# Kernel tuning notes

Hardware: AMD Instinct MI355X
Metric: run time of the kernel (lower is better)

## Reference

```python
import jax, jax.numpy as jnp
import numpy as np
from jax import lax

EPS = 1e-5  # torch BatchNorm2d default eps


def _bn_relu_conv_res(x, g, bt, m, v, W, b):
    # x: (B,C,h,w). Eval-mode BN + ReLU + 3x3 'same' conv + residual (per region tile).
    y = (x - m[:, None, None]) * (g * lax.rsqrt(v + EPS))[:, None, None] + bt[:, None, None]
    y = jax.nn.relu(y)
    y = lax.conv_general_dilated(y, W, (1, 1), ((1, 1), (1, 1)),
                                 dimension_numbers=('NCHW', 'OIHW', 'NCHW'))
    return y + b[None, :, None, None] + x

_tile_fn = jax.vmap(_bn_relu_conv_res)  # vmap over the leading tile axis


def _flat77(p):
    return p[:7, :7].reshape((49,) + p.shape[2:])


def _region_layer(x, g, bt, m, v, W, b):
    # grid=(8,8): torch.split(split_size=H//7) -> 7 tiles of size s and one remainder tile r per axis.
    B, C, H, _ = x.shape
    s = H // 7          # 18 for H=132
    r = H - 7 * s       # 6
    # interior 7x7 tiles (s x s), batched in one vmapped conv
    xi = x[:, :, :7 * s, :7 * s].reshape(B, C, 7, s, 7, s).transpose(2, 4, 0, 1, 3, 5).reshape(49, B, C, s, s)
    oi = _tile_fn(xi, _flat77(g), _flat77(bt), _flat77(m), _flat77(v), _flat77(W), _flat77(b))
    oi = oi.reshape(7, 7, B, C, s, s).transpose(2, 3, 0, 4, 1, 5).reshape(B, C, 7 * s, 7 * s)
    # right column tiles (s x r), j = 7
    xr = x[:, :, :7 * s, 7 * s:].reshape(B, C, 7, s, r).transpose(2, 0, 1, 3, 4)
    orr = _tile_fn(xr, g[:7, 7], bt[:7, 7], m[:7, 7], v[:7, 7], W[:7, 7], b[:7, 7])
    orr = orr.transpose(1, 2, 0, 3, 4).reshape(B, C, 7 * s, r)
    # bottom row tiles (r x s), i = 7
    xb = x[:, :, 7 * s:, :7 * s].reshape(B, C, r, 7, s).transpose(3, 0, 1, 2, 4)
    ob = _tile_fn(xb, g[7, :7], bt[7, :7], m[7, :7], v[7, :7], W[7, :7], b[7, :7])
    ob = ob.transpose(1, 2, 3, 0, 4).reshape(B, C, r, 7 * s)
    # corner tile (r x r)
    oc = _bn_relu_conv_res(x[:, :, 7 * s:, 7 * s:], g[7, 7], bt[7, 7], m[7, 7], v[7, 7], W[7, 7], b[7, 7])
    return jnp.concatenate([jnp.concatenate([oi, orr], 3), jnp.concatenate([ob, oc], 3)], 2)


def _conv(x, W, b, stride):
    y = lax.conv_general_dilated(x, W, (stride, stride), 'VALID',
                                 dimension_numbers=('NCHW', 'OIHW', 'NCHW'))
    return y + b[None, :, None, None]


def _maxpool2(x):
    return lax.reduce_window(x, -jnp.inf, lax.max, (1, 1, 2, 2), (1, 1, 2, 2), 'VALID')


def _bn(x, g, bt, m, v):
    return (x - m[:, None, None]) * (g * lax.rsqrt(v + EPS))[:, None, None] + bt[:, None, None]


def _forward(x, conv1_w, conv1_b, rg_g, rg_b, rg_m, rg_v, rg_w, rg_cb,
             bn2_g, bn2_b, bn2_m, bn2_v, conv2_w, conv2_b, conv3_w, conv3_b,
             conv4_w, conv4_b, conv5_w, conv5_b, fc1_w, fc1_b, fc2_w, fc2_b, fc3_w, fc3_b):
    h = _conv(x, conv1_w, conv1_b, 1)                 # (B,32,132,132)
    h = _region_layer(h, rg_g, rg_b, rg_m, rg_v, rg_w, rg_cb)
    h = jax.nn.relu(h)
    h = _maxpool2(h)                                  # (B,32,66,66)
    h = _bn(h, bn2_g, bn2_b, bn2_m, bn2_v)
    h = jax.nn.relu(_conv(h, conv2_w, conv2_b, 1))    # (B,16,59,59)
    h = jax.nn.relu(_conv(h, conv3_w, conv3_b, 1))    # (B,16,52,52)
    h = jax.nn.relu(_conv(h, conv4_w, conv4_b, 2))    # (B,16,24,24)
    h = jax.nn.relu(_conv(h, conv5_w, conv5_b, 1))    # (B,16,20,20)
    h = h.reshape(h.shape[0], -1)                     # (B,6400)
    h = jax.nn.relu(h @ fc1_w.T + fc1_b)              # dropout = identity (eval)
    h = jax.nn.relu(h @ fc2_w.T + fc2_b)
    return h @ fc3_w.T + fc3_b                        # (B,12)


def setup_inputs() -> dict:
    key = jax.random.key(0)
    ks = jax.random.split(key, 32)
    n = lambda i, shape, s=0.05: s * jax.random.normal(ks[i], shape, jnp.float32)
    B = 64
    return {
        'x': jax.random.normal(ks[0], (B, 3, 142, 142), jnp.float32),
        'conv1_w': n(1, (32, 3, 11, 11)),
        'conv1_b': n(2, (32,), 0.01),
        'rg_g': 1.0 + n(3, (8, 8, 32), 0.1),
        'rg_b': n(4, (8, 8, 32), 0.1),
        'rg_m': n(5, (8, 8, 32), 0.1),
        'rg_v': 1.0 + n(6, (8, 8, 32), 0.1),
        'rg_w': n(7, (8, 8, 32, 32, 3, 3)),
        'rg_cb': n(8, (8, 8, 32), 0.01),
        'bn2_g': 1.0 + n(9, (32,), 0.1),
        'bn2_b': n(10, (32,), 0.1),
        'bn2_m': n(11, (32,), 0.1),
        'bn2_v': 1.0 + n(12, (32,), 0.1),
        'conv2_w': n(13, (16, 32, 8, 8)),
        'conv2_b': n(14, (16,), 0.01),
        'conv3_w': n(15, (16, 16, 8, 8)),
        'conv3_b': n(16, (16,), 0.01),
        'conv4_w': n(17, (16, 16, 6, 6)),
        'conv4_b': n(18, (16,), 0.01),
        'conv5_w': n(19, (16, 16, 5, 5)),
        'conv5_b': n(20, (16,), 0.01),
        'fc1_w': n(21, (4096, 6400), 0.01),
        'fc1_b': n(22, (4096,), 0.01),
        'fc2_w': n(23, (2048, 4096), 0.01),
        'fc2_b': n(24, (2048,), 0.01),
        'fc3_w': n(25, (12, 2048), 0.01),
        'fc3_b': n(26, (12,), 0.01),
    }


def reference(x, conv1_w, conv1_b, rg_g, rg_b, rg_m, rg_v, rg_w, rg_cb,
              bn2_g, bn2_b, bn2_m, bn2_v, conv2_w, conv2_b, conv3_w, conv3_b,
              conv4_w, conv4_b, conv5_w, conv5_b, fc1_w, fc1_b, fc2_w, fc2_b, fc3_w, fc3_b):
    return _forward(x, conv1_w, conv1_b, rg_g, rg_b, rg_m, rg_v, rg_w, rg_cb,
                    bn2_g, bn2_b, bn2_m, bn2_v, conv2_w, conv2_b, conv3_w, conv3_b,
                    conv4_w, conv4_b, conv5_w, conv5_b, fc1_w, fc1_b, fc2_w, fc2_b, fc3_w, fc3_b)
```

## Files before the change

### kernel.cpp

```cpp
#include <hip/hip_runtime.h>

#define EPS 1e-5f

typedef __attribute__((ext_vector_type(4)))  __bf16 bf16x4;
typedef __attribute__((ext_vector_type(8)))  __bf16 bf16x8;
typedef __attribute__((ext_vector_type(4)))  float  f32x4;
typedef __attribute__((ext_vector_type(16))) float  f32x16;

template <int TH, int TW, int NIMG>
__device__ void fused_body(const float* __restrict__ xg,
                           const float* __restrict__ c1w, const float* __restrict__ c1b,
                           const float* __restrict__ gg, const float* __restrict__ bb,
                           const float* __restrict__ mm, const float* __restrict__ vv,
                           const float* __restrict__ ww, const float* __restrict__ cbp,
                           const float* __restrict__ g2, const float* __restrict__ b2,
                           const float* __restrict__ m2, const float* __restrict__ v2,
                           __bf16* __restrict__ hp,
                           __bf16* act, __bf16* wlds1, __bf16* sx, __bf16* zbuf,
                           float* prm,
                           int reg, int n0, int Y0, int X0)
{
    constexpr int C     = TW + 10;
    constexpr int RR    = TH + 10;
    constexpr int SSTR  = 4 * (TH + 11);
    constexpr int NP    = TH * TW;
    constexpr int NPT   = (NP + 31) / 32;
    constexpr int NT    = (NPT + 3) / 4;
    constexpr int PWW   = TW / 2;
    constexpr int TOT   = 3 * RR * C;
    constexpr int NLOAD = (TOT + 255) / 256;

    const int tid  = threadIdx.x;
    const int lane = tid & 63;
    const int wv   = tid >> 6;
    const int half = lane >> 5;
    const int l31  = lane & 31;
    const int YP = Y0 >> 1, XP = X0 >> 1;

    if (tid < 32) {
        const float sc = gg[reg * 32 + tid] * rsqrtf(vv[reg * 32 + tid] + EPS);
        const float b1 = c1b[tid];
        prm[tid]       = sc;
        prm[32 + tid]  = bb[reg * 32 + tid] - mm[reg * 32 + tid] * sc + sc * b1;
        prm[64 + tid]  = cbp[reg * 32 + tid] + b1;
        const float s2 = g2[tid] * rsqrtf(v2[tid] + EPS);
        prm[96 + tid]  = s2;
        prm[128 + tid] = b2[tid] - m2[tid] * s2;
    }
    for (int i = tid; i < 16896; i += 256) {
        const int j = i & 7, co = (i >> 3) & 31, hf = (i >> 8) & 1, cc = i >> 9;
        const int c = cc % 3, kx = cc / 3;
        const int k48 = c * 16 + hf * 8 + j, ky = k48 >> 2, ci = k48 & 3;
        const float v = (ci < 3 && ky < 11) ? c1w[((co * 3 + ci) * 11 + ky) * 11 + kx] : 0.f;
        wlds1[i] = (__bf16)v;
    }
    for (int i = tid; i < 9216; i += 256) {
        const int co = i / 288, r = i - co * 288;
        const int ci = r / 9, tap = r - ci * 9;
        act[((tap * 4 + (ci >> 3)) * 32 + co) * 8 + (ci & 7)] = (__bf16)ww[(long)reg * 9216 + i];
    }
    for (int i = tid; i < C * SSTR; i += 256) sx[i] = (__bf16)0.f;
    __syncthreads();

    bf16x8 afrag[18];
    #pragma unroll
    for (int c = 0; c < 18; ++c) {
        const int tap = c >> 1;
        const int grp = (c & 1) * 2 + half;
        afrag[c] = *(const bf16x8*)&act[((tap * 4 + grp) * 32 + l31) * 8];
    }

    const int sub = l31 & 3;
    int py[NT], px[NT], yy0[NT], xx0[NT]; bool val[NT];
    #pragma unroll
    for (int t = 0; t < NT; ++t) {
        const int til = wv + t * 4;
        int p = til * 32 + l31;
        val[t] = (til < NPT) && (p < NP);
        if (!val[t]) p = l31;
        const int q = p >> 2;
        py[t] = q / PWW; px[t] = q - py[t] * PWW;
        yy0[t] = 2 * py[t] + ((p & 3) >> 1);
        xx0[t] = 2 * px[t] + (p & 1);
    }

    float pf[NLOAD];
    #pragma unroll
    for (int k = 0; k < NLOAD; ++k) {
        const int idx = tid + k * 256;
        float v = 0.f;
        if (idx < TOT) {
            const int col = idx % C, rr = idx / C;
            const int row = rr % RR, ci = rr / RR;
            v = xg[(((long)n0 * 3 + ci) * 142 + Y0 + row) * 142 + X0 + col];
        }
        pf[k] = v;
    }
    __syncthreads();

    for (int img = 0; img < NIMG; ++img) {
        const int n = n0 + img;
        #pragma unroll
        for (int k = 0; k < NLOAD; ++k) {
            const int idx = tid + k * 256;
            if (idx < TOT) {
                const int col = idx % C, rr = idx / C;
                const int row = rr % RR, ci = rr / RR;
                sx[col * SSTR + row * 4 + ci] = (__bf16)pf[k];
            }
        }
        __syncthreads();
        if (img + 1 < NIMG) {
            #pragma unroll
            for (int k = 0; k < NLOAD; ++k) {
                const int idx = tid + k * 256;
                if (idx < TOT) {
                    const int col = idx % C, rr = idx / C;
                    const int row = rr % RR, ci = rr / RR;
                    pf[k] = xg[(((long)(n + 1) * 3 + ci) * 142 + Y0 + row) * 142 + X0 + col];
                }
            }
        }
        f32x16 a1[NT];
        #pragma unroll
        for (int t = 0; t < NT; ++t) a1[t] = (f32x16){};
        for (int kx = 0; kx < 11; ++kx) {
            #pragma unroll
            for (int c = 0; c < 3; ++c) {
                const bf16x8 A = *(const bf16x8*)&wlds1[(((kx * 3 + c) * 2 + half) * 32 + l31) * 8];
                #pragma unroll
                for (int t = 0; t < NT; ++t) {
                    if (wv + t * 4 < NPT) {
                        const int off = (xx0[t] + kx) * SSTR + (yy0[t] + c * 4 + half * 2) * 4;
                        const bf16x4 lo = *(const bf16x4*)&sx[off];
                        const bf16x4 hi = *(const bf16x4*)&sx[off + 4];
                        a1[t] = __builtin_amdgcn_mfma_f32_32x32x16_bf16(
                                    A, __builtin_shufflevector(lo, hi, 0, 1, 2, 3, 4, 5, 6, 7),
                                    a1[t], 0, 0, 0);
                    }
                }
            }
        }
        #pragma unroll
        for (int t = 0; t < NT; ++t) {
            if (val[t]) {
                const int pix = yy0[t] * TW + xx0[t];
                #pragma unroll
                for (int g = 0; g < 4; ++g) {
                    bf16x4 pk;
                    #pragma unroll
                    for (int j = 0; j < 4; ++j) {
                        const int co = 4 * half + 8 * g + j;
                        pk[j] = (__bf16)fmaxf(a1[t][4 * g + j] * prm[co] + prm[32 + co], 0.f);
                    }
                    *(bf16x4*)&act[pix * 36 + 8 * g + 4 * half] = pk;
                }
            }
        }
        __syncthreads();
        f32x16 ar[NT];
        #pragma unroll
        for (int t = 0; t < NT; ++t) ar[t] = a1[t];
        #pragma unroll
        for (int c = 0; c < 18; ++c) {
            const int tap = c >> 1;
            const int ky = tap / 3, kxx = tap - ky * 3;
            #pragma unroll
            for (int t = 0; t < NT; ++t) {
                if (wv + t * 4 < NPT) {
                    const int yy = yy0[t] + ky - 1, xx = xx0[t] + kxx - 1;
                    const bool in = ((unsigned)yy < (unsigned)TH) && ((unsigned)xx < (unsigned)TW);
                    const __bf16* src = in ? &act[(yy * TW + xx) * 36 + (c & 1) * 16 + half * 8] : zbuf;
                    const bf16x4 lo = *(const bf16x4*)src;
                    const bf16x4 hi = *(const bf16x4*)(src + 4);
                    ar[t] = __builtin_amdgcn_mfma_f32_32x32x16_bf16(
                                afrag[c], __builtin_shufflevector(lo, hi, 0, 1, 2, 3, 4, 5, 6, 7),
                                ar[t], 0, 0, 0);
                }
            }
        }
        #pragma unroll
        for (int t = 0; t < NT; ++t) {
            if (wv + t * 4 < NPT) {
                #pragma unroll
                for (int r = 0; r < 16; ++r) {
                    const int co = (r & 3) + 8 * (r >> 2) + 4 * half;
                    float v = ar[t][r] + prm[64 + co];
                    v = fmaxf(v, 0.f);
                    v = fmaxf(v, __shfl_xor(v, 1));
                    v = fmaxf(v, __shfl_xor(v, 2));
                    if (val[t] && sub == 0) {
                        hp[(((long)n * 32 + co) * 66 + YP + py[t]) * 66 + XP + px[t]]
                            = (__bf16)(v * prm[96 + co] + prm[128 + co]);
                    }
                }
            }
        }
    }
}

__global__ __launch_bounds__(256, 2) void k_fused(const float* __restrict__ xg,
                                                  const float* __restrict__ c1w,
                                                  const float* __restrict__ c1b,
                                                  const float* __restrict__ gg,
                                                  const float* __restrict__ bb,
                                                  const float* __restrict__ mm,
                                                  const float* __restrict__ vv,
                                                  const float* __restrict__ ww,
                                                  const float* __restrict__ cbp,
                                                  const float* __restrict__ g2,
                                                  const float* __restrict__ b2,
                                                  const float* __restrict__ m2,
                                                  const float* __restrict__ v2,
                                                  __bf16* __restrict__ hp)
{
    __shared__ __align__(16) __bf16 act[11664];
    __shared__ __align__(16) __bf16 wlds1[16896];
    __shared__ __align__(16) __bf16 sx[3248];
    __shared__ __align__(16) __bf16 zbuf[8];
    __shared__ float prm[160];
    if (threadIdx.x < 8) zbuf[threadIdx.x] = (__bf16)0.f;
    const int reg = blockIdx.x;
    const int ri = reg >> 3, rj = reg & 7;
    const int n0 = blockIdx.y * 8;
    const int Y0 = ri * 18, X0 = rj * 18;
    if (ri < 7 && rj < 7)
        fused_body<18, 18, 8>(xg, c1w, c1b, gg, bb, mm, vv, ww, cbp, g2, b2, m2, v2, hp,
                              act, wlds1, sx, zbuf, prm, reg, n0, Y0, X0);
    else if (ri < 7)
        fused_body<18, 6, 8>(xg, c1w, c1b, gg, bb, mm, vv, ww, cbp, g2, b2, m2, v2, hp,
                             act, wlds1, sx, zbuf, prm, reg, n0, Y0, X0);
    else if (rj < 7)
        fused_body<6, 18, 8>(xg, c1w, c1b, gg, bb, mm, vv, ww, cbp, g2, b2, m2, v2, hp,
                             act, wlds1, sx, zbuf, prm, reg, n0, Y0, X0);
    else
        fused_body<6, 6, 8>(xg, c1w, c1b, gg, bb, mm, vv, ww, cbp, g2, b2, m2, v2, hp,
                            act, wlds1, sx, zbuf, prm, reg, n0, Y0, X0);
}

__global__ void k_wprep(const float* __restrict__ w, __bf16* __restrict__ wA,
                        int CIN, int KS, int NCHUNK)
{
    const int NG = CIN / 16;
    const int total = NG * NCHUNK * 512;
    const int i = blockIdx.x * 256 + threadIdx.x;
    if (i >= total) return;
    const int j   = i & 7;
    const int co  = (i >> 3) & 15;
    const int quad = (i >> 7) & 3;
    const int ch  = (i >> 9) % NCHUNK;
    const int g   = (i >> 9) / NCHUNK;
    const int k   = ch * 32 + quad * 8 + j;
    const int t   = k >> 4, c = k & 15;
    float v = 0.f;
    if (t < KS * KS) v = w[((co * CIN + g * 16 + c) * KS + t / KS) * KS + t % KS];
    wA[i] = (__bf16)v;
}

template <typename TIN, typename TOUT, int CIN, int KS, int HIN, int HOUT, int R>
__global__ __launch_bounds__(256) void k_conv_mfma(const TIN* __restrict__ in,
                                                   const __bf16* __restrict__ wA,
                                                   const float* __restrict__ bias,
                                                   TOUT* __restrict__ out)
{
    constexpr int NG     = CIN / 16;
    constexpr int TAPS   = KS * KS;
    constexpr int NCHUNK = (TAPS * 16 + 31) / 32;
    constexpr int NROWS  = R + KS - 1;
    constexpr int NP     = R * HOUT;
    constexpr int NTIL   = (NP + 15) / 16;
    constexpr int NT     = (NTIL + 3) / 4;
    __shared__ __align__(16) __bf16 act[NROWS * HIN * 20];
    __shared__ __align__(16) __bf16 wl[NCHUNK * 512];
    const int tid  = threadIdx.x;
    const int lane = tid & 63;
    const int wv   = tid >> 6;
    const int quad = lane >> 4;
    const int m    = lane & 15;
    const int n    = blockIdx.y;
    int y0 = blockIdx.x * R; if (y0 > HOUT - R) y0 = HOUT - R;

    int yl[NT], xx[NT]; bool val[NT];
    #pragma unroll
    for (int t = 0; t < NT; ++t) {
        const int til = wv + t * 4;
        int p = til * 16 + m;
        val[t] = (til < NTIL) && (p < NP);
        if (!val[t]) p = m;
        yl[t] = p / HOUT; xx[t] = p - yl[t] * HOUT;
    }
    f32x4 acc[NT];
    #pragma unroll
    for (int t = 0; t < NT; ++t) acc[t] = (f32x4){0.f, 0.f, 0.f, 0.f};

    for (int g = 0; g < NG; ++g) {
        if (g) __syncthreads();
        for (int i = tid; i < NCHUNK * 256; i += 256)
            ((unsigned*)wl)[i] = ((const unsigned*)wA)[g * NCHUNK * 256 + i];
        for (int i = tid; i < 16 * NROWS * HIN; i += 256) {
            const int c = i / (NROWS * HIN), px = i - c * (NROWS * HIN);
            const int r = px / HIN, xc = px - r * HIN;
            act[px * 20 + c] = (__bf16)in[(((long)n * CIN + g * 16 + c) * HIN + y0 + r) * HIN + xc];
        }
        __syncthreads();
        for (int ch = 0; ch < NCHUNK; ++ch) {
            const bf16x8 a = *(const bf16x8*)&wl[(ch * 4 + quad) * 128 + m * 8];
            const int kbase = ch * 32 + quad * 8;
            int t = kbase >> 4;
            const int c0 = kbase & 15;
            int ky = 0, kx = 0;
            if (t < TAPS) { ky = t / KS; kx = t - ky * KS; }
            #pragma unroll
            for (int tt = 0; tt < NT; ++tt) {
                const int off = ((yl[tt] + ky) * HIN + xx[tt] + kx) * 20 + c0;
                const bf16x4 lo = *(const bf16x4*)&act[off];
                const bf16x4 hi = *(const bf16x4*)&act[off + 4];
                const bf16x8 b = __builtin_shufflevector(lo, hi, 0, 1, 2, 3, 4, 5, 6, 7);
                acc[tt] = __builtin_amdgcn_mfma_f32_16x16x32_bf16(a, b, acc[tt], 0, 0, 0);
            }
        }
    }
    #pragma unroll
    for (int tt = 0; tt < NT; ++tt) {
        if (!val[tt]) continue;
        #pragma unroll
        for (int r = 0; r < 4; ++r) {
            const int co = quad * 4 + r;
            out[(((long)n * 16 + co) * HOUT + y0 + yl[tt]) * HOUT + xx[tt]]
                = (TOUT)fmaxf(acc[tt][r] + bias[co], 0.f);
        }
    }
}

template <int CIN, int KS, int STRIDE, int HIN, int HOUT>
__global__ __launch_bounds__(256) void k_conv(const float* __restrict__ in,
                                              const float* __restrict__ w,
                                              const float* __restrict__ bias,
                                              __bf16* __restrict__ out)
{
    const int co = blockIdx.y, n = blockIdx.z;
    constexpr int GR  = (HOUT + 3) / 4;
    constexpr int WSZ = CIN * KS * KS;
    constexpr int LEN = KS + 3 * STRIDE;
    __shared__ float ws[WSZ];
    for (int i = threadIdx.x; i < WSZ; i += 256) ws[i] = w[co * WSZ + i];
    __syncthreads();
    const int g = blockIdx.x * 256 + threadIdx.x;
    if (g >= HOUT * GR) return;
    const int y = g / GR;
    int x0 = (g - y * GR) * 4;
    if (x0 > HOUT - 4) x0 = HOUT - 4;
    float a0 = bias[co], a1 = a0, a2 = a0, a3 = a0;
    const float* base = in + (long)n * CIN * HIN * HIN;
    for (int ci = 0; ci < CIN; ++ci) {
        for (int ky = 0; ky < KS; ++ky) {
            const float* row = base + ((long)ci * HIN + y * STRIDE + ky) * HIN + x0 * STRIDE;
            float r[LEN];
            #pragma unroll
            for (int i = 0; i < LEN; ++i) r[i] = row[i];
            const float* wr = ws + (ci * KS + ky) * KS;
            #pragma unroll
            for (int kx = 0; kx < KS; ++kx) {
                const float wv = wr[kx];
                a0 = fmaf(wv, r[kx],              a0);
                a1 = fmaf(wv, r[kx + STRIDE],     a1);
                a2 = fmaf(wv, r[kx + 2 * STRIDE], a2);
                a3 = fmaf(wv, r[kx + 3 * STRIDE], a3);
            }
        }
    }
    __bf16* o = out + (((long)n * 16 + co) * HOUT + y) * HOUT + x0;
    o[0] = (__bf16)fmaxf(a0, 0.f); o[1] = (__bf16)fmaxf(a1, 0.f);
    o[2] = (__bf16)fmaxf(a2, 0.f); o[3] = (__bf16)fmaxf(a3, 0.f);
}

__global__ __launch_bounds__(256) void k_fc2(const float* __restrict__ A,
                                             const float* __restrict__ W,
                                             float* __restrict__ C,
                                             int N, int K, int kchunk)
{
    __shared__ float As[64][68];
    __shared__ float Bs[64][132];
    const int n0 = blockIdx.x * 128;
    const int kbeg = blockIdx.y * kchunk;
    const int tid = threadIdx.x;
    const int tm = tid >> 4, tn = tid & 15;
    const int am = tid >> 2, ac = tid & 3;
    const int bn = tid >> 1, bh = tid & 1;
    float acc[4][8] = {};
    for (int k0 = kbeg; k0 < kbeg + kchunk; k0 += 64) {
        #pragma unroll
        for (int q = 0; q < 4; ++q) {
            const int kk = ac * 16 + q * 4;
            const float4 v = *(const float4*)&A[(long)am * K + k0 + kk];
            As[kk + 0][am] = v.x; As[kk + 1][am] = v.y;
            As[kk + 2][am] = v.z; As[kk + 3][am] = v.w;
        }
        const int nn = n0 + bn;
        if (nn < N) {
            #pragma unroll
            for (int q = 0; q < 8; ++q) {
                const int kk = bh * 32 + q * 4;
                const float4 v = *(const float4*)&W[(long)nn * K + k0 + kk];
                Bs[kk + 0][bn] = v.x; Bs[kk + 1][bn] = v.y;
                Bs[kk + 2][bn] = v.z; Bs[kk + 3][bn] = v.w;
            }
        }
        __syncthreads();
        #pragma unroll 4
        for (int kk = 0; kk < 64; ++kk) {
            float a[4], b[8];
            #pragma unroll
            for (int i = 0; i < 4; ++i) a[i] = As[kk][tm * 4 + i];
            #pragma unroll
            for (int j = 0; j < 8; ++j) b[j] = Bs[kk][tn * 8 + j];
            #pragma unroll
            for (int i = 0; i < 4; ++i)
                #pragma unroll
                for (int j = 0; j < 8; ++j)
                    acc[i][j] = fmaf(a[i], b[j], acc[i][j]);
        }
        __syncthreads();
    }
    #pragma unroll
    for (int i = 0; i < 4; ++i) {
        const int m = tm * 4 + i;
        #pragma unroll
        for (int j = 0; j < 8; ++j) {
            const int nn = n0 + tn * 8 + j;
            if (nn < N) atomicAdd(&C[(long)m * N + nn], acc[i][j]);
        }
    }
}

__global__ __launch_bounds__(256) void k_bias_act(const float* __restrict__ C,
                                                  const float* __restrict__ bias,
                                                  float* __restrict__ out,
                                                  int N, int total, int relu)
{
    const int i = blockIdx.x * 256 + threadIdx.x;
    if (i >= total) return;
    float v = C[i] + bias[i % N];
    if (relu) v = fmaxf(v, 0.f);
    out[i] = v;
}

extern "C" void kernel_launch(void* const* d_in, const int* in_sizes, int n_in,
                              void* d_out, int out_size, void* d_ws, size_t ws_size,
                              hipStream_t stream)
{
    (void)in_sizes; (void)n_in; (void)out_size; (void)ws_size;
    const float* x       = (const float*)d_in[0];
    const float* conv1_w = (const float*)d_in[1];
    const float* conv1_b = (const float*)d_in[2];
    const float* rg_g    = (const float*)d_in[3];
    const float* rg_b    = (const float*)d_in[4];
    const float* rg_m    = (const float*)d_in[5];
    const float* rg_v    = (const float*)d_in[6];
    const float* rg_w    = (const float*)d_in[7];
    const float* rg_cb   = (const float*)d_in[8];
    const float* bn2_g   = (const float*)d_in[9];
    const float* bn2_b   = (const float*)d_in[10];
    const float* bn2_m   = (const float*)d_in[11];
    const float* bn2_v   = (const float*)d_in[12];
    const float* conv2_w = (const float*)d_in[13];
    const float* conv2_b = (const float*)d_in[14];
    const float* conv3_w = (const float*)d_in[15];
    const float* conv3_b = (const float*)d_in[16];
    const float* conv4_w = (const float*)d_in[17];
    const float* conv4_b = (const float*)d_in[18];
    const float* conv5_w = (const float*)d_in[19];
    const float* conv5_b = (const float*)d_in[20];
    const float* fc1_w   = (const float*)d_in[21];
    const float* fc1_b   = (const float*)d_in[22];
    const float* fc2_w   = (const float*)d_in[23];
    const float* fc2_b   = (const float*)d_in[24];
    const float* fc3_w   = (const float*)d_in[25];
    const float* fc3_b   = (const float*)d_in[26];

    float* ws = (float*)d_ws;
    __bf16* hp  = (__bf16*)ws;
    float*  b2f = ws + 4460544;
    __bf16* wA2 = (__bf16*)(b2f);
    __bf16* wA3 = (__bf16*)(b2f + 16384);
    __bf16* wA5 = (__bf16*)(b2f + 24576);
    __bf16* h3  = (__bf16*)(b2f + 27904);
    float*  h4  = b2f + 27904 + 1782272;
    __bf16* h5  = (__bf16*)(h4 + 2768896);
    float*  h6  = (float*)h5 + 294912;
    float*  f1  = h6 + 409600;
    float*  f2  = f1 + 262144;
    float*  f3  = f2 + 131072;

    k_fused<<<dim3(64, 8), 256, 0, stream>>>(x, conv1_w, conv1_b,
                                             rg_g, rg_b, rg_m, rg_v, rg_w, rg_cb,
                                             bn2_g, bn2_b, bn2_m, bn2_v, hp);

    k_wprep<<<dim3(128), 256, 0, stream>>>(conv2_w, wA2, 32, 8, 32);
    k_wprep<<<dim3(64), 256, 0, stream>>>(conv3_w, wA3, 16, 8, 32);
    k_wprep<<<dim3(26), 256, 0, stream>>>(conv5_w, wA5, 16, 5, 13);

    k_conv_mfma<__bf16, __bf16, 32, 8, 66, 59, 4><<<dim3(15, 64), 256, 0, stream>>>(hp, wA2, conv2_b, h3);
    k_conv_mfma<__bf16, float, 16, 8, 59, 52, 4><<<dim3(13, 64), 256, 0, stream>>>(h3, wA3, conv3_b, h4);
    k_conv<16, 6, 2, 52, 24><<<dim3(1, 16, 64), 256, 0, stream>>>(h4, conv4_w, conv4_b, h5);
    k_conv_mfma<__bf16, float, 16, 5, 24, 20, 10><<<dim3(2, 64), 256, 0, stream>>>(h5, wA5, conv5_b, h6);

    hipMemsetAsync(f1, 0, 262144 * sizeof(float), stream);
    k_fc2<<<dim3(32, 10), 256, 0, stream>>>(h6, fc1_w, f1, 4096, 6400, 640);
    k_bias_act<<<dim3((262144 + 255) / 256), 256, 0, stream>>>(f1, fc1_b, f1, 4096, 262144, 1);

    hipMemsetAsync(f2, 0, 131072 * sizeof(float), stream);
    k_fc2<<<dim3(16, 16), 256, 0, stream>>>(f1, fc2_w, f2, 2048, 4096, 256);
    k_bias_act<<<dim3((131072 + 255) / 256), 256, 0, stream>>>(f2, fc2_b, f2, 2048, 131072, 1);

    hipMemsetAsync(f3, 0, 768 * sizeof(float), stream);
    k_fc2<<<dim3(1, 16), 256, 0, stream>>>(f2, fc3_w, f3, 12, 2048, 128);
    k_bias_act<<<dim3(3), 256, 0, stream>>>(f3, fc3_b, (float*)d_out, 12, 768, 0);
}
```

Before: 751.9 us.

## Precompute all weights once, switch intermediates to channels-last, cut LDS and raise occupancy

Adds one k_wprep_all kernel that converts the conv1, region, conv2, conv3 and conv5 weights into MFMA-ready bf16 layouts in global memory. The fused and conv kernels now read A fragments directly from global/L1 instead of staging them in LDS, which frees shared memory and lets launch bounds ask for 4 blocks per CU. The fused kernel's pooled output and conv2's output become channels-last so the next conv can do 16-byte vector loads, and LDS strides are padded to 40 and 24 so B operands load as single bf16x8. Images per fused block drop from 8 to 4 (more blocks), and conv5 rows per block drop from 10 to 5. The risks are extra global-memory weight reads inside the MFMA loops and register pressure under the tighter launch bounds.

After: 766.9 us. +2.0%, slower.

```diff
diff --git a/kernel.cpp b/kernel.cpp
--- a/kernel.cpp
+++ b/kernel.cpp
@@ -7,17 +7,67 @@
 typedef __attribute__((ext_vector_type(4)))  float  f32x4;
 typedef __attribute__((ext_vector_type(16))) float  f32x16;
 
+__device__ inline void wprep_generic(const float* __restrict__ w, __bf16* __restrict__ wA,
+                                     int CIN, int KS, int NCHUNK, int i)
+{
+    const int j    = i & 7;
+    const int co   = (i >> 3) & 15;
+    const int quad = (i >> 7) & 3;
+    const int ch   = (i >> 9) % NCHUNK;
+    const int g    = (i >> 9) / NCHUNK;
+    const int k    = ch * 32 + quad * 8 + j;
+    const int t    = k >> 4, c = k & 15;
+    float v = 0.f;
+    if (t < KS * KS) v = w[((co * CIN + g * 16 + c) * KS + t / KS) * KS + t % KS];
+    wA[i] = (__bf16)v;
+}
+
+__global__ __launch_bounds__(256) void k_wprep_all(const float* __restrict__ c1w,
+                                                   const float* __restrict__ rgw,
+                                                   const float* __restrict__ w2,
+                                                   const float* __restrict__ w3,
+                                                   const float* __restrict__ w5,
+                                                   __bf16* __restrict__ wA1,
+                                                   __bf16* __restrict__ wR,
+                                                   __bf16* __restrict__ wA2,
+                                                   __bf16* __restrict__ wA3,
+                                                   __bf16* __restrict__ wA5)
+{
+    int i = blockIdx.x * 256 + threadIdx.x;
+    if (i < 16896) {
+        const int j = i & 7, co = (i >> 3) & 31, hf = (i >> 8) & 1, grp = i >> 9;
+        const int kx = grp / 3, c = grp - kx * 3;
+        const int k48 = c * 16 + hf * 8 + j, ky = k48 >> 2, ci = k48 & 3;
+        wA1[i] = (__bf16)((ci < 3 && ky < 11) ? c1w[((co * 3 + ci) * 11 + ky) * 11 + kx] : 0.f);
+        return;
+    }
+    i -= 16896;
+    if (i < 589824) {
+        const int reg = i / 9216, q = i - reg * 9216;
+        const int j = q & 7, co = (q >> 3) & 31, cg = (q >> 8) & 3, tap = q >> 10;
+        const int ci = cg * 8 + j;
+        wR[i] = (__bf16)rgw[(size_t)reg * 9216 + co * 288 + ci * 9 + tap];
+        return;
+    }
+    i -= 589824;
+    if (i < 32768) { wprep_generic(w2, wA2, 32, 8, 32, i); return; }
+    i -= 32768;
+    if (i < 16384) { wprep_generic(w3, wA3, 16, 8, 32, i); return; }
+    i -= 16384;
+    if (i < 6656)  { wprep_generic(w5, wA5, 16, 5, 13, i); }
+}
+
 template <int TH, int TW, int NIMG>
 __device__ void fused_body(const float* __restrict__ xg,
-                           const float* __restrict__ c1w, const float* __restrict__ c1b,
+                           const __bf16* __restrict__ wA1, const __bf16* __restrict__ wR,
+                           const float* __restrict__ c1b,
                            const float* __restrict__ gg, const float* __restrict__ bb,
                            const float* __restrict__ mm, const float* __restrict__ vv,
-                           const float* __restrict__ ww, const float* __restrict__ cbp,
+                           const float* __restrict__ cbp,
                            const float* __restrict__ g2, const float* __restrict__ b2,
                            const float* __restrict__ m2, const float* __restrict__ v2,
                            __bf16* __restrict__ hp,
-                           __bf16* act, __bf16* wlds1, __bf16* sx, __bf16* zbuf,
-                           float* prm,
+                           __bf16* act, __bf16* sx, __bf16* zbuf, float* prm,
                            int reg, int n0, int Y0, int X0)
 {
     constexpr int C     = TW + 10;
@@ -29,6 +79,7 @@
     constexpr int PWW   = TW / 2;
     constexpr int TOT   = 3 * RR * C;
     constexpr int NLOAD = (TOT + 255) / 256;
+    constexpr int ASTR  = 40;
 
     const int tid  = threadIdx.x;
     const int lane = tid & 63;
@@ -47,28 +98,9 @@
         prm[96 + tid]  = s2;
         prm[128 + tid] = b2[tid] - m2[tid] * s2;
     }
-    for (int i = tid; i < 16896; i += 256) {
-        const int j = i & 7, co = (i >> 3) & 31, hf = (i >> 8) & 1, cc = i >> 9;
-        const int c = cc % 3, kx = cc / 3;
-        const int k48 = c * 16 + hf * 8 + j, ky = k48 >> 2, ci = k48 & 3;
-        const float v = (ci < 3 && ky < 11) ? c1w[((co * 3 + ci) * 11 + ky) * 11 + kx] : 0.f;
-        wlds1[i] = (__bf16)v;
-    }
-    for (int i = tid; i < 9216; i += 256) {
-        const int co = i / 288, r = i - co * 288;
-        const int ci = r / 9, tap = r - ci * 9;
-        act[((tap * 4 + (ci >> 3)) * 32 + co) * 8 + (ci & 7)] = (__bf16)ww[(long)reg * 9216 + i];
-    }
     for (int i = tid; i < C * SSTR; i += 256) sx[i] = (__bf16)0.f;
-    __syncthreads();
-
-    bf16x8 afrag[18];
-    #pragma unroll
-    for (int c = 0; c < 18; ++c) {
-        const int tap = c >> 1;
-        const int grp = (c & 1) * 2 + half;
-        afrag[c] = *(const bf16x8*)&act[((tap * 4 + grp) * 32 + l31) * 8];
-    }
+
+    const __bf16* wRr = wR + (size_t)reg * 9216;
 
     const int sub = l31 & 3;
     int py[NT], px[NT], yy0[NT], xx0[NT]; bool val[NT];
@@ -92,7 +124,7 @@
         if (idx < TOT) {
             const int col = idx % C, rr = idx / C;
             const int row = rr % RR, ci = rr / RR;
-            v = xg[(((long)n0 * 3 + ci) * 142 + Y0 + row) * 142 + X0 + col];
+            v = xg[(((size_t)n0 * 3 + ci) * 142 + Y0 + row) * 142 + X0 + col];
         }
         pf[k] = v;
     }
@@ -117,7 +149,7 @@
                 if (idx < TOT) {
                     const int col = idx % C, rr = idx / C;
                     const int row = rr % RR, ci = rr / RR;
-                    pf[k] = xg[(((long)(n + 1) * 3 + ci) * 142 + Y0 + row) * 142 + X0 + col];
+                    pf[k] = xg[(((size_t)(n + 1) * 3 + ci) * 142 + Y0 + row) * 142 + X0 + col];
                 }
             }
         }
@@ -127,7 +159,7 @@
         for (int kx = 0; kx < 11; ++kx) {
             #pragma unroll
             for (int c = 0; c < 3; ++c) {
-                const bf16x8 A = *(const bf16x8*)&wlds1[(((kx * 3 + c) * 2 + half) * 32 + l31) * 8];
+                const bf16x8 A = *(const bf16x8*)&wA1[((kx * 3 + c) * 2 + half) * 256 + l31 * 8];
                 #pragma unroll
                 for (int t = 0; t < NT; ++t) {
                     if (wv + t * 4 < NPT) {
@@ -153,7 +185,7 @@
                         const int co = 4 * half + 8 * g + j;
                         pk[j] = (__bf16)fmaxf(a1[t][4 * g + j] * prm[co] + prm[32 + co], 0.f);
                     }
-                    *(bf16x4*)&act[pix * 36 + 8 * g + 4 * half] = pk;
+                    *(bf16x4*)&act[pix * ASTR + 8 * g + 4 * half] = pk;
                 }
             }
         }
@@ -165,23 +197,22 @@
         for (int c = 0; c < 18; ++c) {
             const int tap = c >> 1;
             const int ky = tap / 3, kxx = tap - ky * 3;
+            const bf16x8 A = *(const bf16x8*)&wRr[(tap * 4 + (c & 1) * 2 + half) * 256 + l31 * 8];
             #pragma unroll
             for (int t = 0; t < NT; ++t) {
                 if (wv + t * 4 < NPT) {
                     const int yy = yy0[t] + ky - 1, xx = xx0[t] + kxx - 1;
                     const bool in = ((unsigned)yy < (unsigned)TH) && ((unsigned)xx < (unsigned)TW);
-                    const __bf16* src = in ? &act[(yy * TW + xx) * 36 + (c & 1) * 16 + half * 8] : zbuf;
-                    const bf16x4 lo = *(const bf16x4*)src;
-                    const bf16x4 hi = *(const bf16x4*)(src + 4);
-                    ar[t] = __builtin_amdgcn_mfma_f32_32x32x16_bf16(
-                                afrag[c], __builtin_shufflevector(lo, hi, 0, 1, 2, 3, 4, 5, 6, 7),
-                                ar[t], 0, 0, 0);
+                    const __bf16* src = in ? &act[(yy * TW + xx) * ASTR + (c & 1) * 16 + half * 8] : zbuf;
+                    const bf16x8 B = *(const bf16x8*)src;
+                    ar[t] = __builtin_amdgcn_mfma_f32_32x32x16_bf16(A, B, ar[t], 0, 0, 0);
                 }
             }
         }
         #pragma unroll
         for (int t = 0; t < NT; ++t) {
             if (wv + t * 4 < NPT) {
+                float pooled[16];
                 #pragma unroll
                 for (int r = 0; r < 16; ++r) {
                     const int co = (r & 3) + 8 * (r >> 2) + 4 * half;
@@ -189,9 +220,19 @@
                     v = fmaxf(v, 0.f);
                     v = fmaxf(v, __shfl_xor(v, 1));
                     v = fmaxf(v, __shfl_xor(v, 2));
-                    if (val[t] && sub == 0) {
-                        hp[(((long)n * 32 + co) * 66 + YP + py[t]) * 66 + XP + px[t]]
-                            = (__bf16)(v * prm[96 + co] + prm[128 + co]);
+                    pooled[r] = v;
+                }
+                if (val[t] && sub == 0) {
+                    const size_t base = (((size_t)n * 66 + YP + py[t]) * 66 + XP + px[t]) * 32;
+                    #pragma unroll
+                    for (int g = 0; g < 4; ++g) {
+                        bf16x4 pk;
+                        #pragma unroll
+                        for (int j = 0; j < 4; ++j) {
+                            const int co = 8 * g + 4 * half + j;
+                            pk[j] = (__bf16)(pooled[g * 4 + j] * prm[96 + co] + prm[128 + co]);
+                        }
+                        *(bf16x4*)&hp[base + 8 * g + 4 * half] = pk;
                     }
                 }
             }
@@ -199,14 +240,14 @@
     }
 }
 
-__global__ __launch_bounds__(256, 2) void k_fused(const float* __restrict__ xg,
-                                                  const float* __restrict__ c1w,
+__global__ __launch_bounds__(256, 4) void k_fused(const float* __restrict__ xg,
+                                                  const __bf16* __restrict__ wA1,
+                                                  const __bf16* __restrict__ wR,
                                                   const float* __restrict__ c1b,
                                                   const float* __restrict__ gg,
                                                   const float* __restrict__ bb,
                                                   const float* __restrict__ mm,
                                                   const float* __restrict__ vv,
-                                                  const float* __restrict__ ww,
                                                   const float* __restrict__ cbp,
                                                   const float* __restrict__ g2,
                                                   const float* __restrict__ b2,
@@ -214,54 +255,35 @@
                                                   const float* __restrict__ v2,
                                                   __bf16* __restrict__ hp)
 {
-    __shared__ __align__(16) __bf16 act[11664];
-    __shared__ __align__(16) __bf16 wlds1[16896];
+    __shared__ __align__(16) __bf16 act[12960];
     __shared__ __align__(16) __bf16 sx[3248];
     __shared__ __align__(16) __bf16 zbuf[8];
     __shared__ float prm[160];
     if (threadIdx.x < 8) zbuf[threadIdx.x] = (__bf16)0.f;
     const int reg = blockIdx.x;
     const int ri = reg >> 3, rj = reg & 7;
-    const int n0 = blockIdx.y * 8;
+    const int n0 = blockIdx.y * 4;
     const int Y0 = ri * 18, X0 = rj * 18;
     if (ri < 7 && rj < 7)
-        fused_body<18, 18, 8>(xg, c1w, c1b, gg, bb, mm, vv, ww, cbp, g2, b2, m2, v2, hp,
-                              act, wlds1, sx, zbuf, prm, reg, n0, Y0, X0);
+        fused_body<18, 18, 4>(xg, wA1, wR, c1b, gg, bb, mm, vv, cbp, g2, b2, m2, v2, hp,
+                              act, sx, zbuf, prm, reg, n0, Y0, X0);
     else if (ri < 7)
-        fused_body<18, 6, 8>(xg, c1w, c1b, gg, bb, mm, vv, ww, cbp, g2, b2, m2, v2, hp,
-                             act, wlds1, sx, zbuf, prm, reg, n0, Y0, X0);
+        fused_body<18, 6, 4>(xg, wA1, wR, c1b, gg, bb, mm, vv, cbp, g2, b2, m2, v2, hp,
+                             act, sx, zbuf, prm, reg, n0, Y0, X0);
     else if (rj < 7)
-        fused_body<6, 18, 8>(xg, c1w, c1b, gg, bb, mm, vv, ww, cbp, g2, b2, m2, v2, hp,
-                             act, wlds1, sx, zbuf, prm, reg, n0, Y0, X0);
+        fused_body<6, 18, 4>(xg, wA1, wR, c1b, gg, bb, mm, vv, cbp, g2, b2, m2, v2, hp,
+                             act, sx, zbuf, prm, reg, n0, Y0, X0);
     else
-        fused_body<6, 6, 8>(xg, c1w, c1b, gg, bb, mm, vv, ww, cbp, g2, b2, m2, v2, hp,
-                            act, wlds1, sx, zbuf, prm, reg, n0, Y0, X0);
-}
-
-__global__ void k_wprep(const float* __restrict__ w, __bf16* __restrict__ wA,
-                        int CIN, int KS, int NCHUNK)
-{
-    const int NG = CIN / 16;
-    const int total = NG * NCHUNK * 512;
-    const int i = blockIdx.x * 256 + threadIdx.x;
-    if (i >= total) return;
-    const int j   = i & 7;
-    const int co  = (i >> 3) & 15;
-    const int quad = (i >> 7) & 3;
-    const int ch  = (i >> 9) % NCHUNK;
-    const int g   = (i >> 9) / NCHUNK;
-    const int k   = ch * 32 + quad * 8 + j;
-    const int t   = k >> 4, c = k & 15;
-    float v = 0.f;
-    if (t < KS * KS) v = w[((co * CIN + g * 16 + c) * KS + t / KS) * KS + t % KS];
-    wA[i] = (__bf16)v;
-}
-
-template <typename TIN, typename TOUT, int CIN, int KS, int HIN, int HOUT, int R>
-__global__ __launch_bounds__(256) void k_conv_mfma(const TIN* __restrict__ in,
-                                                   const __bf16* __restrict__ wA,
-                                                   const float* __restrict__ bias,
-                                                   TOUT* __restrict__ out)
+        fused_body<6, 6, 4>(xg, wA1, wR, c1b, gg, bb, mm, vv, cbp, g2, b2, m2, v2, hp,
+                            act, sx, zbuf, prm, reg, n0, Y0, X0);
+}
+
+template <typename TIN, typename TOUT, int CIN, int KS, int HIN, int HOUT, int R,
+          bool INCL, bool OUTCL>
+__global__ __launch_bounds__(256, 4) void k_conv_mfma(const TIN* __restrict__ in,
+                                                      const __bf16* __restrict__ wA,
+                                                      const float* __restrict__ bias,
+                                                      TOUT* __restrict__ out)
 {
     constexpr int NG     = CIN / 16;
     constexpr int TAPS   = KS * KS;
@@ -270,8 +292,7 @@
     constexpr int NP     = R * HOUT;
     constexpr int NTIL   = (NP + 15) / 16;
     constexpr int NT     = (NTIL + 3) / 4;
-    __shared__ __align__(16) __bf16 act[NROWS * HIN * 20];
-    __shared__ __align__(16) __bf16 wl[NCHUNK * 512];
+    __shared__ __align__(16) __bf16 act[NROWS * HIN * 24];
     const int tid  = threadIdx.x;
     const int lane = tid & 63;
     const int wv   = tid >> 6;
@@ -295,16 +316,23 @@
 
     for (int g = 0; g < NG; ++g) {
         if (g) __syncthreads();
-        for (int i = tid; i < NCHUNK * 256; i += 256)
-            ((unsigned*)wl)[i] = ((const unsigned*)wA)[g * NCHUNK * 256 + i];
-        for (int i = tid; i < 16 * NROWS * HIN; i += 256) {
-            const int c = i / (NROWS * HIN), px = i - c * (NROWS * HIN);
-            const int r = px / HIN, xc = px - r * HIN;
-            act[px * 20 + c] = (__bf16)in[(((long)n * CIN + g * 16 + c) * HIN + y0 + r) * HIN + xc];
+        if constexpr (INCL) {
+            for (int u = tid; u < NROWS * HIN * 2; u += 256) {
+                const int px = u >> 1, hlf = u & 1;
+                const int r = px / HIN, xc = px - r * HIN;
+                const bf16x8 v = *(const bf16x8*)&in[(((size_t)n * HIN + y0 + r) * HIN + xc) * CIN + g * 16 + hlf * 8];
+                *(bf16x8*)&act[px * 24 + hlf * 8] = v;
+            }
+        } else {
+            for (int i = tid; i < 16 * NROWS * HIN; i += 256) {
+                const int c = i / (NROWS * HIN), px = i - c * (NROWS * HIN);
+                const int r = px / HIN, xc = px - r * HIN;
+                act[px * 24 + c] = (__bf16)in[(((size_t)n * CIN + g * 16 + c) * HIN + y0 + r) * HIN + xc];
+            }
         }
         __syncthreads();
         for (int ch = 0; ch < NCHUNK; ++ch) {
-            const bf16x8 a = *(const bf16x8*)&wl[(ch * 4 + quad) * 128 + m * 8];
+            const bf16x8 a = *(const bf16x8*)&wA[(size_t)g * NCHUNK * 512 + (ch * 4 + quad) * 128 + m * 8];
             const int kbase = ch * 32 + quad * 8;
             int t = kbase >> 4;
             const int c0 = kbase & 15;
@@ -312,10 +340,8 @@
             if (t < TAPS) { ky = t / KS; kx = t - ky * KS; }
             #pragma unroll
             for (int tt = 0; tt < NT; ++tt) {
-                const int off = ((yl[tt] + ky) * HIN + xx[tt] + kx) * 20 + c0;
-                const bf16x4 lo = *(const bf16x4*)&act[off];
-                const bf16x4 hi = *(const bf16x4*)&act[off + 4];
-                const bf16x8 b = __builtin_shufflevector(lo, hi, 0, 1, 2, 3, 4, 5, 6, 7);
+                const int off = ((yl[tt] + ky) * HIN + xx[tt] + kx) * 24 + c0;
+                const bf16x8 b = *(const bf16x8*)&act[off];
                 acc[tt] = __builtin_amdgcn_mfma_f32_16x16x32_bf16(a, b, acc[tt], 0, 0, 0);
             }
         }
@@ -323,11 +349,19 @@
     #pragma unroll
     for (int tt = 0; tt < NT; ++tt) {
         if (!val[tt]) continue;
-        #pragma unroll
-        for (int r = 0; r < 4; ++r) {
-            const int co = quad * 4 + r;
-            out[(((long)n * 16 + co) * HOUT + y0 + yl[tt]) * HOUT + xx[tt]]
-                = (TOUT)fmaxf(acc[tt][r] + bias[co], 0.f);
+        if constexpr (OUTCL) {
+            bf16x4 pk;
+            #pragma unroll
+            for (int r = 0; r < 4; ++r)
+                pk[r] = (__bf16)fmaxf(acc[tt][r] + bias[quad * 4 + r], 0.f);
+            *(bf16x4*)&out[(((size_t)n * HOUT + y0 + yl[tt]) * HOUT + xx[tt]) * 16 + quad * 4] = pk;
+        } else {
+            #pragma unroll
+            for (int r = 0; r < 4; ++r) {
+                const int co = quad * 4 + r;
+                out[(((size_t)n * 16 + co) * HOUT + y0 + yl[tt]) * HOUT + xx[tt]]
+                    = (TOUT)fmaxf(acc[tt][r] + bias[co], 0.f);
+            }
         }
     }
 }
@@ -351,10 +385,10 @@
     int x0 = (g - y * GR) * 4;
     if (x0 > HOUT - 4) x0 = HOUT - 4;
     float a0 = bias[co], a1 = a0, a2 = a0, a3 = a0;
-    const float* base = in + (long)n * CIN * HIN * HIN;
+    const float* base = in + (size_t)n * CIN * HIN * HIN;
     for (int ci = 0; ci < CIN; ++ci) {
         for (int ky = 0; ky < KS; ++ky) {
-            const float* row = base + ((long)ci * HIN + y * STRIDE + ky) * HIN + x0 * STRIDE;
+            const float* row = base + ((size_t)ci * HIN + y * STRIDE + ky) * HIN + x0 * STRIDE;
             float r[LEN];
             #pragma unroll
             for (int i = 0; i < LEN; ++i) r[i] = row[i];
@@ -369,7 +403,7 @@
             }
         }
     }
-    __bf16* o = out + (((long)n * 16 + co) * HOUT + y) * HOUT + x0;
+    __bf16* o = out + (((size_t)n * 16 + co) * HOUT + y) * HOUT + x0;
     o[0] = (__bf16)fmaxf(a0, 0.f); o[1] = (__bf16)fmaxf(a1, 0.f);
     o[2] = (__bf16)fmaxf(a2, 0.f); o[3] = (__bf16)fmaxf(a3, 0.f);
 }
@@ -392,7 +426,7 @@
         #pragma unroll
         for (int q = 0; q < 4; ++q) {
             const int kk = ac * 16 + q * 4;
-            const float4 v = *(const float4*)&A[(long)am * K + k0 + kk];
+            const float4 v = *(const float4*)&A[(size_t)am * K + k0 + kk];
             As[kk + 0][am] = v.x; As[kk + 1][am] = v.y;
             As[kk + 2][am] = v.z; As[kk + 3][am] = v.w;
         }
@@ -401,7 +435,7 @@
             #pragma unroll
             for (int q = 0; q < 8; ++q) {
                 const int kk = bh * 32 + q * 4;
-                const float4 v = *(const float4*)&W[(long)nn * K + k0 + kk];
+                const float4 v = *(const float4*)&W[(size_t)nn * K + k0 + kk];
                 Bs[kk + 0][bn] = v.x; Bs[kk + 1][bn] = v.y;
                 Bs[kk + 2][bn] = v.z; Bs[kk + 3][bn] = v.w;
             }
@@ -424,11 +458,11 @@
     }
     #pragma unroll
     for (int i = 0; i < 4; ++i) {
-        const int m = tm * 4 + i;
+        const int mi = tm * 4 + i;
         #pragma unroll
         for (int j = 0; j < 8; ++j) {
             const int nn = n0 + tn * 8 + j;
-            if (nn < N) atomicAdd(&C[(long)m * N + nn], acc[i][j]);
+            if (nn < N) atomicAdd(&C[(size_t)mi * N + nn], acc[i][j]);
         }
     }
 }
@@ -480,30 +514,30 @@
 
     float* ws = (float*)d_ws;
     __bf16* hp  = (__bf16*)ws;
-    float*  b2f = ws + 4460544;
-    __bf16* wA2 = (__bf16*)(b2f);
-    __bf16* wA3 = (__bf16*)(b2f + 16384);
-    __bf16* wA5 = (__bf16*)(b2f + 24576);
-    __bf16* h3  = (__bf16*)(b2f + 27904);
-    float*  h4  = b2f + 27904 + 1782272;
-    __bf16* h5  = (__bf16*)(h4 + 2768896);
-    float*  h6  = (float*)h5 + 294912;
-    float*  f1  = h6 + 409600;
-    float*  f2  = f1 + 262144;
-    float*  f3  = f2 + 131072;
-
-    k_fused<<<dim3(64, 8), 256, 0, stream>>>(x, conv1_w, conv1_b,
-                                             rg_g, rg_b, rg_m, rg_v, rg_w, rg_cb,
-                                             bn2_g, bn2_b, bn2_m, bn2_v, hp);
-
-    k_wprep<<<dim3(128), 256, 0, stream>>>(conv2_w, wA2, 32, 8, 32);
-    k_wprep<<<dim3(64), 256, 0, stream>>>(conv3_w, wA3, 16, 8, 32);
-    k_wprep<<<dim3(26), 256, 0, stream>>>(conv5_w, wA5, 16, 5, 13);
-
-    k_conv_mfma<__bf16, __bf16, 32, 8, 66, 59, 4><<<dim3(15, 64), 256, 0, stream>>>(hp, wA2, conv2_b, h3);
-    k_conv_mfma<__bf16, float, 16, 8, 59, 52, 4><<<dim3(13, 64), 256, 0, stream>>>(h3, wA3, conv3_b, h4);
+    __bf16* wA1 = (__bf16*)(ws + 4460544);
+    __bf16* wR  = (__bf16*)(ws + 4468992);
+    __bf16* wA2 = (__bf16*)(ws + 4763904);
+    __bf16* wA3 = (__bf16*)(ws + 4780288);
+    __bf16* wA5 = (__bf16*)(ws + 4788480);
+    __bf16* h3  = (__bf16*)(ws + 4791808);
+    float*  h4  = ws + 6574080;
+    __bf16* h5  = (__bf16*)(ws + 9342976);
+    float*  h6  = ws + 9637888;
+    float*  f1  = ws + 10047488;
+    float*  f2  = ws + 10309632;
+    float*  f3  = ws + 10440704;
+
+    k_wprep_all<<<dim3(2588), 256, 0, stream>>>(conv1_w, rg_w, conv2_w, conv3_w, conv5_w,
+                                                wA1, wR, wA2, wA3, wA5);
+
+    k_fused<<<dim3(64, 16), 256, 0, stream>>>(x, wA1, wR, conv1_b,
+                                              rg_g, rg_b, rg_m, rg_v, rg_cb,
+                                              bn2_g, bn2_b, bn2_m, bn2_v, hp);
+
+    k_conv_mfma<__bf16, __bf16, 32, 8, 66, 59, 4, true,  true ><<<dim3(15, 64), 256, 0, stream>>>(hp, wA2, conv2_b, h3);
+    k_conv_mfma<__bf16, float,  16, 8, 59, 52, 4, true,  false><<<dim3(13, 64), 256, 0, stream>>>(h3, wA3, conv3_b, h4);
     k_conv<16, 6, 2, 52, 24><<<dim3(1, 16, 64), 256, 0, stream>>>(h4, conv4_w, conv4_b, h5);
-    k_conv_mfma<__bf16, float, 16, 5, 24, 20, 10><<<dim3(2, 64), 256, 0, stream>>>(h5, wA5, conv5_b, h6);
+    k_conv_mfma<__bf16, float,  16, 5, 24, 20, 5, false, false><<<dim3(4, 64), 256, 0, stream>>>(h5, wA5, conv5_b, h6);
 
     hipMemsetAsync(f1, 0, 262144 * sizeof(float), stream);
     k_fc2<<<dim3(32, 10), 256, 0, stream>>>(h6, fc1_w, f1, 4096, 6400, 640);
```
